# Kernel tuning notes

Measured on AMD Instinct MI355X. Metric: run time of the kernel, lower is better.

The kernel has to match this reference:

```python
import jax, jax.numpy as jnp
import numpy as np
from jax import lax

N_QUBITS = 4   # in_channels * kernel_size^2 = 1*2*2
N_LAYERS = 2
K = 2
STRIDE = 1


def _bshape(theta, N):
    # broadcast scalar or (N,) angle to (N, 1, 1, ..., 1) for statevector broadcasting
    return jnp.broadcast_to(theta, (N,)).reshape((N,) + (1,) * N_QUBITS)


def _rx(state, theta, w):
    # RX(theta) on wire w (axis w+1): cos(t/2) I - i sin(t/2) X
    N = state.shape[0]
    c = _bshape(jnp.cos(theta * 0.5), N)
    s = _bshape(jnp.sin(theta * 0.5), N)
    return c * state - 1j * s * jnp.flip(state, axis=w + 1)


def _rz(state, theta, w):
    # RZ(theta): phase e^{-i t/2} on |0>, e^{+i t/2} on |1> of wire w
    N = state.shape[0]
    sgn = jnp.array([-0.5, 0.5], dtype=state.real.dtype).reshape(
        (1,) * (w + 1) + (2,) + (1,) * (N_QUBITS - 1 - w))
    return state * jnp.exp(1j * (_bshape(theta, N) * sgn))


def _cnot(state, control, target):
    ca, ta = control + 1, target + 1
    s0 = jnp.take(state, 0, axis=ca)
    s1 = jnp.take(state, 1, axis=ca)
    ta2 = ta if ta < ca else ta - 1
    s1 = jnp.flip(s1, axis=ta2)
    return jnp.stack([s0, s1], axis=ca)


def _simulate(angles, params):
    # angles: (N, n_qubits) float32; params: (n_layers, n_qubits, 2)
    N = angles.shape[0]
    state = jnp.zeros((N,) + (2,) * N_QUBITS, dtype=jnp.complex64)
    state = state.at[(slice(None),) + (0,) * N_QUBITS].set(1.0)
    # AngleEmbedding: RX(x_w) on wire w
    for w in range(N_QUBITS):
        state = _rx(state, angles[:, w], w)
    # quantum_circuit_1
    for l in range(N_LAYERS):
        for w in range(N_QUBITS):
            state = _rx(state, params[l, w, 0], w)
            state = _rz(state, params[l, w, 1], w)
        for w in range(N_QUBITS - 1):
            # qml.CNOT(wires=[w+1, w]) -> control w+1, target w
            state = _cnot(state, w + 1, w)
    probs = state.real ** 2 + state.imag ** 2  # (N, 2,...,2)
    zs = []
    for w in range(N_QUBITS):
        other = tuple(a for a in range(1, N_QUBITS + 1) if a != w + 1)
        m = probs.sum(axis=other)  # (N, 2)
        zs.append(m[:, 0] - m[:, 1])
    return jnp.stack(zs, axis=1)  # (N, n_qubits)


def _forward(x, params):
    B, C, H, W = x.shape
    Ho = (H - K) // STRIDE + 1
    Wo = (W - K) // STRIDE + 1
    # (B, C*K*K, Ho, Wo); feature dim flattened channel-major (C, kh, kw),
    # matching torch.flatten(input[:, :, i:i+k, j:j+k], start_dim=1)
    patches = lax.conv_general_dilated_patches(x, (K, K), (STRIDE, STRIDE), 'VALID')
    angles = patches.transpose(0, 2, 3, 1).reshape(-1, N_QUBITS)  # (B*Ho*Wo, nq)
    z = _simulate(angles, params)  # (B*Ho*Wo, nq)
    return z.reshape(B, Ho, Wo, N_QUBITS).transpose(0, 3, 1, 2)  # (B, nq, Ho, Wo)


def setup_inputs() -> dict:
    key = jax.random.key(0)
    k1, k2 = jax.random.split(key)
    x = jax.random.uniform(k1, (32, 1, 128, 128), dtype=jnp.float32)
    params = jax.random.uniform(k2, (N_LAYERS, N_QUBITS, 2), dtype=jnp.float32)
    return {"x": x, "params": params}


def reference(x, params):
    return _forward(x, params)
```

## Files before the change

### kernel.cpp

```cpp
#include <hip/hip_runtime.h>


#define HH 128
#define WW 128
#define HO 127
#define WO 127
#define BB 32

template <int M>
__device__ __forceinline__ void rx_gate(float* re, float* im, float th) {
    float s, c;
    __sincosf(th * 0.5f, &s, &c);
#pragma unroll
    for (int idx = 0; idx < 16; ++idx) {
        if (idx & M) continue;
        const int p = idx | M;
        float r0 = re[idx], i0 = im[idx], r1 = re[p], i1 = im[p];
        re[idx] = fmaf(c, r0, s * i1);
        im[idx] = fmaf(c, i0, -s * r1);
        re[p]   = fmaf(c, r1, s * i0);
        im[p]   = fmaf(c, i1, -s * r0);
    }
}

template <int M>
__device__ __forceinline__ void rz_gate(float* re, float* im, float th) {
    float sp, cp;
    __sincosf(th * 0.5f, &sp, &cp);
#pragma unroll
    for (int idx = 0; idx < 16; ++idx) {
        float r = re[idx], q = im[idx];
        if (idx & M) {
            re[idx] = fmaf(r, cp, -q * sp);
            im[idx] = fmaf(q, cp, r * sp);
        } else {
            re[idx] = fmaf(r, cp, q * sp);
            im[idx] = fmaf(q, cp, -r * sp);
        }
    }
}

template <int CM, int TM>
__device__ __forceinline__ void cnot_gate(float* re, float* im) {
#pragma unroll
    for (int idx = 0; idx < 16; ++idx) {
        if ((idx & CM) && !(idx & TM)) {
            const int p = idx | TM;
            float t;
            t = re[idx]; re[idx] = re[p]; re[p] = t;
            t = im[idx]; im[idx] = im[p]; im[p] = t;
        }
    }
}

__device__ __forceinline__ void param_circuit(float* re, float* im,
                                              const float* __restrict__ prm) {
#pragma unroll
    for (int l = 0; l < 2; ++l) {
        const float* p = prm + l * 8;
        rx_gate<8>(re, im, p[0]); rz_gate<8>(re, im, p[1]);
        rx_gate<4>(re, im, p[2]); rz_gate<4>(re, im, p[3]);
        rx_gate<2>(re, im, p[4]); rz_gate<2>(re, im, p[5]);
        rx_gate<1>(re, im, p[6]); rz_gate<1>(re, im, p[7]);
        cnot_gate<4, 8>(re, im);
        cnot_gate<2, 4>(re, im);
        cnot_gate<1, 2>(re, im);
    }
}

__global__ __launch_bounds__(384) void qconv_setup(const float* __restrict__ prm,
                                                   float* __restrict__ W) {
    __shared__ float Ur[16][16];
    __shared__ float Ui[16][16];
    const int tid = threadIdx.x;
    if (tid < 16) {
        float re[16], im[16];
#pragma unroll
        for (int k = 0; k < 16; ++k) { re[k] = (k == tid) ? 1.f : 0.f; im[k] = 0.f; }
        param_circuit(re, im, prm);
#pragma unroll
        for (int k = 0; k < 16; ++k) { Ur[k][tid] = re[k]; Ui[k][tid] = im[k]; }
    }
    __syncthreads();
    if (tid < 324) {
        const int w = tid / 81;
        int p = tid % 81;
        const int t3 = p % 3; p /= 3;
        const int t2 = p % 3; p /= 3;
        const int t1 = p % 3;
        const int t0 = p / 3;
        const int f = (t0 == 1 ? 8 : 0) | (t1 == 1 ? 4 : 0) |
                      (t2 == 1 ? 2 : 0) | (t3 == 1 ? 1 : 0);
        const int zbit = 8 >> w;
        float acc = 0.f;
        for (int i = 0; i < 16; ++i) {
            float pr = 1.f, pi = 0.f;
            {
                int ib;
                ib = (i >> 3) & 1;
                if (t0 == 2) { if (ib) { pr = -pr; pi = -pi; } }
                else if (t0 == 1) { float tt = pr; if (ib) { pr = -pi; pi = tt; } else { pr = pi; pi = -tt; } }
                ib = (i >> 2) & 1;
                if (t1 == 2) { if (ib) { pr = -pr; pi = -pi; } }
                else if (t1 == 1) { float tt = pr; if (ib) { pr = -pi; pi = tt; } else { pr = pi; pi = -tt; } }
                ib = (i >> 1) & 1;
                if (t2 == 2) { if (ib) { pr = -pr; pi = -pi; } }
                else if (t2 == 1) { float tt = pr; if (ib) { pr = -pi; pi = tt; } else { pr = pi; pi = -tt; } }
                ib = i & 1;
                if (t3 == 2) { if (ib) { pr = -pr; pi = -pi; } }
                else if (t3 == 1) { float tt = pr; if (ib) { pr = -pi; pi = tt; } else { pr = pi; pi = -tt; } }
            }
            const int j = i ^ f;
            float sr = 0.f, si = 0.f;
            for (int k = 0; k < 16; ++k) {
                float zk = (k & zbit) ? -1.f : 1.f;
                float ar = Ur[k][j], ai = Ui[k][j];
                float br = Ur[k][i], bi = Ui[k][i];
                sr += zk * fmaf(ar, br, ai * bi);
                si += zk * fmaf(ar, bi, -ai * br);
            }
            acc += pr * sr - pi * si;
        }
        W[tid] = acc * (1.0f / 16.0f);
    }
}

__global__ __launch_bounds__(256) void qconv_eval(
    const float* __restrict__ x, const float* __restrict__ W,
    float* __restrict__ out, int total) {
    int tid = blockIdx.x * blockDim.x + threadIdx.x;
    if (tid >= total) return;

    int j = tid % WO;
    int t = tid / WO;
    int i = t % HO;
    int b = t / HO;

    const float* xp = x + ((size_t)b * HH + i) * WW + j;
    float a0 = xp[0], a1 = xp[1], a2 = xp[WW], a3 = xp[WW + 1];

    float s0, c0, s1, c1, s2, c2, s3, c3;
    __sincosf(a0, &s0, &c0);
    __sincosf(a1, &s1, &c1);
    __sincosf(a2, &s2, &c2);
    __sincosf(a3, &s3, &c3);
    const float y0 = -s0, y1 = -s1, y2 = -s2, y3 = -s3;

    float z[4];
#pragma unroll
    for (int w = 0; w < 4; ++w) {
        const float* Ww = W + w * 81;
        float accw = 0.f;
#pragma unroll
        for (int p0 = 0; p0 < 3; ++p0) {
            float b0 = 0.f;
#pragma unroll
            for (int p1 = 0; p1 < 3; ++p1) {
                float b1 = 0.f;
#pragma unroll
                for (int p2 = 0; p2 < 3; ++p2) {
                    const float* q = Ww + ((p0 * 3 + p1) * 3 + p2) * 3;
                    float d = fmaf(c3, q[2], fmaf(y3, q[1], q[0]));
                    if (p2 == 0)      b1 += d;
                    else if (p2 == 1) b1 = fmaf(y2, d, b1);
                    else              b1 = fmaf(c2, d, b1);
                }
                if (p1 == 0)      b0 += b1;
                else if (p1 == 1) b0 = fmaf(y1, b1, b0);
                else              b0 = fmaf(c1, b1, b0);
            }
            if (p0 == 0)      accw += b0;
            else if (p0 == 1) accw = fmaf(y0, b0, accw);
            else              accw = fmaf(c0, b0, accw);
        }
        z[w] = accw;
    }

    float* o = out + (((size_t)b * 4) * HO + (size_t)i) * WO + j;
    o[0]           = z[0];
    o[HO * WO]     = z[1];
    o[2 * HO * WO] = z[2];
    o[3 * HO * WO] = z[3];
}

extern "C" void kernel_launch(void* const* d_in, const int* in_sizes, int n_in,
                              void* d_out, int out_size, void* d_ws, size_t ws_size,
                              hipStream_t stream) {
    const float* x = (const float*)d_in[0];
    const float* prm = (const float*)d_in[1];
    float* out = (float*)d_out;
    float* W = (float*)d_ws;

    qconv_setup<<<1, 384, 0, stream>>>(prm, W);

    const int total = BB * HO * WO;
    const int blocks = (total + 255) / 256;
    qconv_eval<<<blocks, 256, 0, stream>>>(x, W, out, total);
}
```

Measured before the change: 77.76 us.

## Interleave coefficient table as float4, stage in LDS, share monomial products

The setup kernel now writes the 81x4 coefficient table interleaved by qubit so each monomial's four coefficients form one float4. The eval kernel copies the table into shared memory and, for each of the 81 monomials, computes the product of trig terms once and accumulates all four outputs from it. Before, each output was evaluated separately with a nested Horner scheme that read scalar coefficients from global memory. The change aims to cut scalar loads, though the full expansion uses roughly 81*4 FMAs plus product multiplies instead of the Horner form. It also adds a block-wide barrier and a launch-bounds occupancy hint.

Result: no change. 78.01 us (+0.3%).

```diff
diff --git a/kernel.cpp b/kernel.cpp
--- a/kernel.cpp
+++ b/kernel.cpp
@@ -85,6 +85,7 @@
     if (tid < 324) {
         const int w = tid / 81;
         int p = tid % 81;
+        const int pidx = p;
         const int t3 = p % 3; p /= 3;
         const int t2 = p % 3; p /= 3;
         const int t1 = p % 3;
@@ -121,13 +122,20 @@
             }
             acc += pr * sr - pi * si;
         }
-        W[tid] = acc * (1.0f / 16.0f);
-    }
-}
-
-__global__ __launch_bounds__(256) void qconv_eval(
+        W[pidx * 4 + w] = acc * (1.0f / 16.0f);
+    }
+}
+
+__global__ __launch_bounds__(256, 4) void qconv_eval(
     const float* __restrict__ x, const float* __restrict__ W,
     float* __restrict__ out, int total) {
+    __shared__ float4 sW[81];
+    {
+        const float4* Wv = (const float4*)W;
+        for (int k = threadIdx.x; k < 81; k += 256) sW[k] = Wv[k];
+    }
+    __syncthreads();
+
     int tid = blockIdx.x * blockDim.x + threadIdx.x;
     if (tid >= total) return;
 
@@ -144,43 +152,40 @@
     __sincosf(a1, &s1, &c1);
     __sincosf(a2, &s2, &c2);
     __sincosf(a3, &s3, &c3);
-    const float y0 = -s0, y1 = -s1, y2 = -s2, y3 = -s3;
-
-    float z[4];
-#pragma unroll
-    for (int w = 0; w < 4; ++w) {
-        const float* Ww = W + w * 81;
-        float accw = 0.f;
-#pragma unroll
-        for (int p0 = 0; p0 < 3; ++p0) {
-            float b0 = 0.f;
-#pragma unroll
-            for (int p1 = 0; p1 < 3; ++p1) {
-                float b1 = 0.f;
-#pragma unroll
-                for (int p2 = 0; p2 < 3; ++p2) {
-                    const float* q = Ww + ((p0 * 3 + p1) * 3 + p2) * 3;
-                    float d = fmaf(c3, q[2], fmaf(y3, q[1], q[0]));
-                    if (p2 == 0)      b1 += d;
-                    else if (p2 == 1) b1 = fmaf(y2, d, b1);
-                    else              b1 = fmaf(c2, d, b1);
+    const float t0v[3] = {1.f, -s0, c0};
+    const float t1v[3] = {1.f, -s1, c1};
+    const float t2v[3] = {1.f, -s2, c2};
+    const float t3v[3] = {1.f, -s3, c3};
+
+    float acc0 = 0.f, acc1 = 0.f, acc2 = 0.f, acc3 = 0.f;
+#pragma unroll
+    for (int p0 = 0; p0 < 3; ++p0) {
+        const float g0 = t0v[p0];
+#pragma unroll
+        for (int p1 = 0; p1 < 3; ++p1) {
+            const float g01 = g0 * t1v[p1];
+#pragma unroll
+            for (int p2 = 0; p2 < 3; ++p2) {
+                const float g012 = g01 * t2v[p2];
+#pragma unroll
+                for (int p3 = 0; p3 < 3; ++p3) {
+                    const int p = ((p0 * 3 + p1) * 3 + p2) * 3 + p3;
+                    const float g = g012 * t3v[p3];
+                    const float4 q = sW[p];
+                    acc0 = fmaf(g, q.x, acc0);
+                    acc1 = fmaf(g, q.y, acc1);
+                    acc2 = fmaf(g, q.z, acc2);
+                    acc3 = fmaf(g, q.w, acc3);
                 }
-                if (p1 == 0)      b0 += b1;
-                else if (p1 == 1) b0 = fmaf(y1, b1, b0);
-                else              b0 = fmaf(c1, b1, b0);
             }
-            if (p0 == 0)      accw += b0;
-            else if (p0 == 1) accw = fmaf(y0, b0, accw);
-            else              accw = fmaf(c0, b0, accw);
-        }
-        z[w] = accw;
+        }
     }
 
     float* o = out + (((size_t)b * 4) * HO + (size_t)i) * WO + j;
-    o[0]           = z[0];
-    o[HO * WO]     = z[1];
-    o[2 * HO * WO] = z[2];
-    o[3 * HO * WO] = z[3];
+    o[0]           = acc0;
+    o[HO * WO]     = acc1;
+    o[2 * HO * WO] = acc2;
+    o[3 * HO * WO] = acc3;
 }
 
 extern "C" void kernel_launch(void* const* d_in, const int* in_sizes, int n_in,
```
